# Kernel tuning notes

Hardware: AMD Instinct MI355X
Metric: run time of the kernel (lower is better)

Reference implementation:

```python
import jax, jax.numpy as jnp
import numpy as np

D_MODEL = 192
D_STATE = 16
D_CONV = 4
EXPAND = 2
HEADDIM = 16
D_INNER = EXPAND * D_MODEL          # 384
NHEADS = D_INNER // HEADDIM         # 24
NGROUPS = 1
CHUNK = 256
BATCH = 2
SEQLEN = 8192
D_IN_PROJ = 2 * D_INNER + NGROUPS * D_STATE + NHEADS   # 808
D_IN_PROJ_B = NGROUPS * D_STATE                         # 16
CONV_DIM = D_INNER + NGROUPS * D_STATE                  # 400
EPS = 1e-5


def silu(x):
    return x * jax.nn.sigmoid(x)


def causal_dwconv(x, w, b):
    # x: (B, L, C), w: (C, 1, K) depthwise, b: (C,). Causal: left-pad K-1.
    C = x.shape[-1]
    xt = jnp.transpose(x, (0, 2, 1))  # (B, C, L)
    y = jax.lax.conv_general_dilated(
        xt, w, window_strides=(1,), padding=[(D_CONV - 1, 0)],
        dimension_numbers=('NCH', 'OIH', 'NCH'), feature_group_count=C)
    return jnp.transpose(y + b[None, :, None], (0, 2, 1))


def segsum(x):
    # x: (..., T) -> (..., T, T) lower-triangular segment sums (exclusive of j, inclusive of i)
    T = x.shape[-1]
    cs = jnp.cumsum(x, axis=-1)
    seg = cs[..., :, None] - cs[..., None, :]
    mask = jnp.tril(jnp.ones((T, T), dtype=bool))
    return jnp.where(mask, seg, -jnp.inf)


def ssd(x, dt, A, Bm, Cm):
    # Mamba2 chunked selective scan (mamba_chunk_scan_combined semantics).
    # x:(b,l,h,p) dt:(b,l,h) A:(h,) Bm,Cm:(b,l,g,n)
    b, l, h, p = x.shape
    g = Bm.shape[2]
    Bm = jnp.repeat(Bm, h // g, axis=2)  # (b,l,h,n)
    Cm = jnp.repeat(Cm, h // g, axis=2)
    nchunks = l // CHUNK
    tochunk = lambda t: t.reshape(b, nchunks, CHUNK, *t.shape[2:])
    xc, dtc, Bc, Cc = map(tochunk, (x, dt, Bm, Cm))
    a = jnp.transpose(dtc * A, (0, 3, 1, 2))        # (b,h,c,cl)
    a_cum = jnp.cumsum(a, axis=-1)                   # (b,h,c,cl)
    Lmat = jnp.exp(segsum(a))                        # (b,h,c,cl,cl)
    xdt = xc * dtc[..., None]                        # (b,c,cl,h,p)
    # intra-chunk (diagonal) output
    Y_diag = jnp.einsum('bclhn,bcshn,bhcls,bcshp->bclhp', Cc, Bc, Lmat, xdt)
    # per-chunk end states
    decay_states = jnp.exp(a_cum[..., -1:] - a_cum)  # (b,h,c,cl)
    states = jnp.einsum('bclhn,bhcl,bclhp->bchpn', Bc, decay_states, xdt)
    # inter-chunk recurrence (associative, via chunk-level segsum)
    init = jnp.zeros_like(states[:, :1])
    states = jnp.concatenate([init, states], axis=1)              # (b,c+1,h,p,n)
    a_chunk = jnp.pad(a_cum[..., -1], ((0, 0), (0, 0), (1, 0)))   # (b,h,c+1)
    decay_chunk = jnp.exp(segsum(a_chunk))                        # (b,h,c+1,c+1)
    states = jnp.einsum('bhzc,bchpn->bzhpn', decay_chunk, states)[:, :-1]  # (b,c,h,p,n)
    # state -> output within each chunk
    Y_off = jnp.einsum('bclhn,bchpn,bhcl->bclhp', Cc, states, jnp.exp(a_cum))
    return (Y_diag + Y_off).reshape(b, l, h, p)


def setup_inputs() -> dict:
    key = jax.random.key(0)
    ks = jax.random.split(key, 12)
    rng = np.random.default_rng(0)
    u = jax.random.normal(ks[0], (BATCH, SEQLEN, D_MODEL), dtype=jnp.float32)
    support = jax.random.normal(ks[1], (BATCH, SEQLEN, D_MODEL), dtype=jnp.float32)
    W_in = jax.random.normal(ks[2], (D_IN_PROJ, D_MODEL), dtype=jnp.float32) * 0.02
    W_in_b = jax.random.normal(ks[3], (D_IN_PROJ_B, D_MODEL), dtype=jnp.float32) * 0.02
    conv_w = jax.random.normal(ks[4], (CONV_DIM, 1, D_CONV), dtype=jnp.float32) * 0.2
    conv_b = jnp.zeros((CONV_DIM,), dtype=jnp.float32)
    conv_w_b = jax.random.normal(ks[5], (D_IN_PROJ_B, 1, D_CONV), dtype=jnp.float32) * 0.2
    conv_b_b = jnp.zeros((D_IN_PROJ_B,), dtype=jnp.float32)
    # dt_bias init per the module (inverse-softplus of dt in [1e-3, 1e-1])
    dt = np.exp(rng.uniform(size=(NHEADS,)) * (np.log(0.1) - np.log(0.001)) + np.log(0.001))
    dt = np.clip(dt, 1e-4, None)
    dt_bias = jnp.asarray(dt + np.log(-np.expm1(-dt)), dtype=jnp.float32)
    A_log = jnp.asarray(np.log(rng.uniform(1.0, 16.0, size=(NHEADS,))), dtype=jnp.float32)
    D = jnp.ones((NHEADS,), dtype=jnp.float32)
    norm_w = jnp.ones((D_INNER,), dtype=jnp.float32)
    W_out = jax.random.normal(ks[6], (D_MODEL, D_INNER), dtype=jnp.float32) * 0.02
    return {'u': u, 'support': support, 'W_in': W_in, 'W_in_b': W_in_b,
            'conv_w': conv_w, 'conv_b': conv_b, 'conv_w_b': conv_w_b, 'conv_b_b': conv_b_b,
            'dt_bias': dt_bias, 'A_log': A_log, 'D': D, 'norm_w': norm_w, 'W_out': W_out}


def reference(u, support, W_in, W_in_b, conv_w, conv_b, conv_w_b, conv_b_b,
              dt_bias, A_log, D, norm_w, W_out):
    bsz, l, _ = u.shape
    zxbdt = u @ W_in.T                                  # (b,l,808)
    c = support @ W_in_b.T                              # (b,l,16)
    z = zxbdt[..., :D_INNER]
    xB = zxbdt[..., D_INNER:D_INNER + CONV_DIM]
    dt = jax.nn.softplus(zxbdt[..., -NHEADS:] + dt_bias)  # (b,l,h)
    A = -jnp.exp(A_log)
    xB = silu(causal_dwconv(xB, conv_w, conv_b))
    Cv = silu(causal_dwconv(c, conv_w_b, conv_b_b))
    x = xB[..., :D_INNER]
    Bv = xB[..., D_INNER:]
    xh = x.reshape(bsz, l, NHEADS, HEADDIM)
    Bg = Bv.reshape(bsz, l, NGROUPS, D_STATE)
    Cg = Cv.reshape(bsz, l, NGROUPS, D_STATE)
    y = ssd(xh, dt, A, Bg, Cg) + D[None, None, :, None] * xh
    y = y.reshape(bsz, l, D_INNER)
    # RMSNormGated, norm_before_gate=False: normalize(y * silu(z)) * weight
    yg = y * silu(z)
    yn = yg * jax.lax.rsqrt(jnp.mean(yg * yg, axis=-1, keepdims=True) + EPS) * norm_w
    return yn @ W_out.T
```

## Files before the change

### kernel.cpp

```cpp
#include <hip/hip_runtime.h>
#include <cmath>

#define ROWS      16384
#define SEQLEN    8192
#define BATCH     2
#define NHEADS    24
#define HEADDIM   16
#define D_STATE   16
#define D_INNER   384
#define D_MODEL   192
#define D_IN_PROJ 808
#define CONV_DIM  400
#define NCHUNKS   32
#define CHUNK     256
#define EPS       1e-5f
#define LOG2E     1.44269504088896f

typedef short bf16x8 __attribute__((ext_vector_type(8)));
typedef float f32x4  __attribute__((ext_vector_type(4)));
typedef unsigned short us4v __attribute__((ext_vector_type(4)));
typedef unsigned short us8v __attribute__((ext_vector_type(8)));

__device__ __forceinline__ float silu_f(float x) { return x / (1.0f + expf(-x)); }
__device__ __forceinline__ float softplus_f(float x) { return (x > 20.0f) ? x : log1pf(expf(x)); }
__device__ __forceinline__ unsigned short f2bf(float x) {
  unsigned u = __builtin_bit_cast(unsigned, x);
  u += 0x7fff + ((u >> 16) & 1);
  return (unsigned short)(u >> 16);
}
__device__ __forceinline__ float bf2f(unsigned short s) {
  unsigned u = (unsigned)s << 16;
  return __builtin_bit_cast(float, u);
}
__device__ __forceinline__ unsigned pk_bf(float a, float b) {
  unsigned ua = __builtin_bit_cast(unsigned, a) + 0x7fffu;
  unsigned ub = __builtin_bit_cast(unsigned, b) + 0x7fffu;
  return __builtin_amdgcn_perm(ub, ua, 0x07060302u);
}

__global__ __launch_bounds__(256)
void cvt3_kernel(const float* __restrict__ a, unsigned short* __restrict__ ao, long na,
                 const float* __restrict__ b, unsigned short* __restrict__ bo, long nb,
                 const float* __restrict__ c, unsigned short* __restrict__ co, long nc) {
  const long t0 = na >> 2, t1 = t0 + (nb >> 2), t2 = t1 + (nc >> 2);
  const long stride = (long)gridDim.x * blockDim.x;
  for (long i = (long)blockIdx.x * blockDim.x + threadIdx.x; i < t2; i += stride) {
    const float4* s; us4v* d; long j;
    if (i < t0)      { s = (const float4*)a; d = (us4v*)ao; j = i; }
    else if (i < t1) { s = (const float4*)b; d = (us4v*)bo; j = i - t0; }
    else             { s = (const float4*)c; d = (us4v*)co; j = i - t1; }
    float4 v = s[j];
    us4v o = { f2bf(v.x), f2bf(v.y), f2bf(v.z), f2bf(v.w) };
    d[j] = o;
  }
}

template<bool A_F32, bool OUT_BF16>
__launch_bounds__(256, 3)
__global__ void gemm_bf16(const void* __restrict__ Ap,
                          const unsigned short* __restrict__ W,
                          void* __restrict__ Cp, int M, int N, int K) {
  constexpr int BM = 128, BN = 128, BK = 32, LDK = 40;
  __shared__ unsigned short As[2][BM * LDK];
  __shared__ unsigned short Ws[2][BN * LDK];
  const int tid  = threadIdx.x;
  const int wid  = tid >> 6, lane = tid & 63;
  const int wr   = wid >> 1, wc = wid & 1;
  const int fr   = lane & 15, fq = lane >> 4;
  const long m0  = (long)blockIdx.y * BM;
  const int  n0  = blockIdx.x * BN;

  f32x4 acc[4][4] = {};

  auto stage = [&](int k0, int buf) {
    if (A_F32) {
      const float* A = (const float*)Ap;
#pragma unroll
      for (int p = 0; p < 2; ++p) {
        int flat = p * 2048 + tid * 8;
        int r = flat >> 5, c = flat & 31;
        const float4* src = (const float4*)(A + (m0 + r) * (long)K + k0 + c);
        float4 v0 = src[0], v1 = src[1];
        us8v o = { f2bf(v0.x), f2bf(v0.y), f2bf(v0.z), f2bf(v0.w),
                   f2bf(v1.x), f2bf(v1.y), f2bf(v1.z), f2bf(v1.w) };
        *(us8v*)&As[buf][r * LDK + c] = o;
      }
    } else {
      const unsigned short* A = (const unsigned short*)Ap;
#pragma unroll
      for (int p = 0; p < 2; ++p) {
        int flat = p * 2048 + tid * 8;
        int r = flat >> 5, c = flat & 31;
        us8v v = *(const us8v*)(A + (m0 + r) * (long)K + k0 + c);
        *(us8v*)&As[buf][r * LDK + c] = v;
      }
    }
#pragma unroll
    for (int p = 0; p < 2; ++p) {
      int flat = p * 2048 + tid * 8;
      int r = flat >> 5, c = flat & 31;
      int gn = n0 + r;
      us8v v = { 0, 0, 0, 0, 0, 0, 0, 0 };
      if (gn < N) v = *(const us8v*)(W + (long)gn * K + k0 + c);
      *(us8v*)&Ws[buf][r * LDK + c] = v;
    }
  };

  const int nk = K / BK;
  stage(0, 0);
  __syncthreads();
  for (int kt = 0; kt < nk; ++kt) {
    const int cur = kt & 1;
    if (kt + 1 < nk) stage((kt + 1) * BK, cur ^ 1);
    bf16x8 af[4], bfr[4];
#pragma unroll
    for (int m = 0; m < 4; ++m)
      af[m] = *(const bf16x8*)&As[cur][(wr * 64 + m * 16 + fr) * LDK + fq * 8];
#pragma unroll
    for (int n = 0; n < 4; ++n)
      bfr[n] = *(const bf16x8*)&Ws[cur][(wc * 64 + n * 16 + fr) * LDK + fq * 8];
#pragma unroll
    for (int m = 0; m < 4; ++m)
#pragma unroll
      for (int n = 0; n < 4; ++n)
        acc[m][n] = __builtin_amdgcn_mfma_f32_16x16x32_bf16(bfr[n], af[m], acc[m][n], 0, 0, 0);
    __syncthreads();
  }

#pragma unroll
  for (int m = 0; m < 4; ++m) {
    const long gm = m0 + wr * 64 + m * 16 + fr;
#pragma unroll
    for (int n = 0; n < 4; ++n) {
      const int gn = n0 + wc * 64 + n * 16 + fq * 4;
      if (gn < N) {
        if (OUT_BF16) {
          us4v o = { f2bf(acc[m][n][0]), f2bf(acc[m][n][1]),
                     f2bf(acc[m][n][2]), f2bf(acc[m][n][3]) };
          *(us4v*)((unsigned short*)Cp + gm * N + gn) = o;
        } else {
          float4 o = make_float4(acc[m][n][0], acc[m][n][1], acc[m][n][2], acc[m][n][3]);
          *(float4*)((float*)Cp + gm * N + gn) = o;
        }
      }
    }
  }
}

#define CBC_NB  (ROWS * 4 / 256)
#define CDT_NB  (ROWS * 3 / 256)

__global__ __launch_bounds__(256)
void conv_bcdt(const unsigned short* __restrict__ zxbdt, const float* __restrict__ cproj,
               const float* __restrict__ conv_w, const float* __restrict__ conv_b,
               const float* __restrict__ conv_w_b, const float* __restrict__ conv_b_b,
               const float* __restrict__ dt_bias,
               unsigned short* __restrict__ Bo, unsigned short* __restrict__ Co,
               float* __restrict__ dtoT) {
  const int blk = blockIdx.x;
  const us8v z8 = { 0, 0, 0, 0, 0, 0, 0, 0 };

  if (blk < CBC_NB) {
    const int idx = blk * 256 + threadIdx.x;
    const int row = idx / 4, q = idx % 4;
    const int b = row / SEQLEN, t = row % SEQLEN;

    if (q < 2) {
      const int c0 = q * 8;
      const unsigned short* base = zxbdt + (size_t)row * D_IN_PROJ + D_INNER + 384 + c0;
      us8v x0 = (t >= 3) ? *(const us8v*)(base - 3 * D_IN_PROJ) : z8;
      us8v x1 = (t >= 2) ? *(const us8v*)(base - 2 * D_IN_PROJ) : z8;
      us8v x2 = (t >= 1) ? *(const us8v*)(base - 1 * D_IN_PROJ) : z8;
      us8v x3 = *(const us8v*)base;
      us8v o;
#pragma unroll
      for (int ch = 0; ch < 8; ++ch) {
        const float4 wv = *(const float4*)(conv_w + (384 + c0 + ch) * 4);
        float acc = conv_b[384 + c0 + ch] + wv.x * bf2f(x0[ch]) + wv.y * bf2f(x1[ch])
                  + wv.z * bf2f(x2[ch]) + wv.w * bf2f(x3[ch]);
        o[ch] = f2bf(silu_f(acc));
      }
      *(us8v*)(Bo + (size_t)row * D_STATE + c0) = o;
    } else {
      const int c0 = (q - 2) * 8;
      const float* base = cproj + (size_t)row * D_STATE + c0;
      float c0r[8], c1r[8], c2r[8], c3r[8];
#pragma unroll
      for (int half = 0; half < 2; ++half) {
        float4 v0 = (t >= 3) ? *(const float4*)(base - 3 * D_STATE + 4 * half) : make_float4(0,0,0,0);
        float4 v1 = (t >= 2) ? *(const float4*)(base - 2 * D_STATE + 4 * half) : make_float4(0,0,0,0);
        float4 v2 = (t >= 1) ? *(const float4*)(base - 1 * D_STATE + 4 * half) : make_float4(0,0,0,0);
        float4 v3 = *(const float4*)(base + 4 * half);
        c0r[4*half+0]=v0.x; c0r[4*half+1]=v0.y; c0r[4*half+2]=v0.z; c0r[4*half+3]=v0.w;
        c1r[4*half+0]=v1.x; c1r[4*half+1]=v1.y; c1r[4*half+2]=v1.z; c1r[4*half+3]=v1.w;
        c2r[4*half+0]=v2.x; c2r[4*half+1]=v2.y; c2r[4*half+2]=v2.z; c2r[4*half+3]=v2.w;
        c3r[4*half+0]=v3.x; c3r[4*half+1]=v3.y; c3r[4*half+2]=v3.z; c3r[4*half+3]=v3.w;
      }
      us8v o;
#pragma unroll
      for (int ch = 0; ch < 8; ++ch) {
        const float4 wv = *(const float4*)(conv_w_b + (c0 + ch) * 4);
        float acc = conv_b_b[c0 + ch] + wv.x * c0r[ch] + wv.y * c1r[ch]
                  + wv.z * c2r[ch] + wv.w * c3r[ch];
        o[ch] = f2bf(silu_f(acc));
      }
      *(us8v*)(Co + (size_t)row * D_STATE + c0) = o;
    }
  } else {
    const int idx = (blk - CBC_NB) * 256 + threadIdx.x;
    const int row = idx / 3, q = idx % 3;
    const int b = row / SEQLEN, t = row % SEQLEN;
    const int h0 = q * 8;
    us8v dv = *(const us8v*)(zxbdt + (size_t)row * D_IN_PROJ + (D_IN_PROJ - NHEADS) + h0);
#pragma unroll
    for (int j = 0; j < 8; ++j) {
      float v = bf2f(dv[j]) + dt_bias[h0 + j];
      dtoT[(size_t)(b * NHEADS + h0 + j) * SEQLEN + t] = softplus_f(v);
    }
  }
}

__global__ __launch_bounds__(512, 4)
void ssd_mfma_kernel(const unsigned short* __restrict__ zxbdt, const unsigned short* __restrict__ Bo,
                     const unsigned short* __restrict__ Co, const float* __restrict__ dtoT,
                     const float* __restrict__ A_log, const float* __restrict__ conv_w,
                     const float* __restrict__ conv_b, const float* __restrict__ Dvec,
                     unsigned short* __restrict__ YdT, float* __restrict__ acum_g,
                     float* __restrict__ csum_g, float* __restrict__ stloc) {
  const int h    = blockIdx.x;
  const int cidx = blockIdx.y;
  const int b    = blockIdx.z;
  const int tid  = threadIdx.x;
  const int wid  = tid >> 6, lane = tid & 63;
  const int fr   = lane & 15, g = lane >> 4;

  __shared__ unsigned short Bs[256 * 24 + 32];
  __shared__ unsigned short xsT[16 * 264];
  __shared__ unsigned short BwT[16 * 264];
  __shared__ unsigned short Ps[8][16 * 40];
  __shared__ unsigned short xraw[259 * 16 + 8];
  __shared__ float sc[CHUNK];
  __shared__ float sc2[CHUNK];
  __shared__ float sred[2][256];
  __shared__ float wsum[4];

  const float Ah = -expf(A_log[h]);
  const us8v z8 = { 0, 0, 0, 0, 0, 0, 0, 0 };

  float v = 0.f;
  if (tid < CHUNK) {
    v = dtoT[(size_t)(b * NHEADS + h) * SEQLEN + (size_t)cidx * CHUNK + tid] * Ah;
#pragma unroll
    for (int off = 1; off < 64; off <<= 1) {
      float u = __shfl_up(v, off, 64);
      if (lane >= off) v += u;
    }
    if (lane == 63) wsum[wid] = v;
  }

  const int r  = tid >> 1;
  const int hf = tid & 1;
  const size_t rrow  = (size_t)b * SEQLEN + (size_t)cidx * CHUNK + r;
  const size_t rhrow = (size_t)(b * NHEADS + h) * SEQLEN + (size_t)cidx * CHUNK + r;
  const float rdtv = dtoT[rhrow];
  us8v bh = ((const us8v*)(Bo + rrow * D_STATE))[hf];
  *(us8v*)&Bs[r * 24 + 8 * hf] = bh;
  if (hf == 0) *(us8v*)&Bs[r * 24 + 16] = z8;
  if (tid < 32) Bs[256 * 24 + tid] = 0;
  {
    const int tg = cidx * CHUNK + r - 3;
    us8v xv = z8;
    if (tg >= 0)
      xv = *(const us8v*)(zxbdt + ((size_t)b * SEQLEN + tg) * D_IN_PROJ + D_INNER + h * HEADDIM + 8 * hf);
    *(us8v*)&xraw[r * 16 + 8 * hf] = xv;
    if (tid < 6) {
      const int rr2 = 256 + (tid >> 1);
      const int hf2 = tid & 1;
      const int tg2 = cidx * CHUNK + rr2 - 3;
      us8v xv2 = *(const us8v*)(zxbdt + ((size_t)b * SEQLEN + tg2) * D_IN_PROJ + D_INNER + h * HEADDIM + 8 * hf2);
      *(us8v*)&xraw[rr2 * 16 + 8 * hf2] = xv2;
    }
  }
  __syncthreads();

  us8v xsil, xdt8;
  {
    us8v tA = *(const us8v*)&xraw[(r + 0) * 16 + 8 * hf];
    us8v tB = *(const us8v*)&xraw[(r + 1) * 16 + 8 * hf];
    us8v tC = *(const us8v*)&xraw[(r + 2) * 16 + 8 * hf];
    us8v tD = *(const us8v*)&xraw[(r + 3) * 16 + 8 * hf];
    const int cbase = h * HEADDIM + 8 * hf;
#pragma unroll
    for (int ch = 0; ch < 8; ++ch) {
      const float4 wv = *(const float4*)(conv_w + (cbase + ch) * 4);
      float acc = conv_b[cbase + ch] + wv.x * bf2f(tA[ch]) + wv.y * bf2f(tB[ch])
                + wv.z * bf2f(tC[ch]) + wv.w * bf2f(tD[ch]);
      float sv = silu_f(acc);
      xsil[ch] = f2bf(sv);
      xdt8[ch] = f2bf(sv * rdtv);
    }
  }
  const float ctot = wsum[0] + wsum[1] + wsum[2] + wsum[3];
  if (tid < CHUNK) {
    float pre = 0.f;
#pragma unroll
    for (int w = 0; w < 4; ++w) if (w < wid) pre += wsum[w];
    v += pre;
    sc[tid]  = v;
    sc2[tid] = v * LOG2E;
    acum_g[(size_t)(b * NHEADS + h) * SEQLEN + (size_t)cidx * CHUNK + tid] = v;
    if (tid == CHUNK - 1) csum_g[(b * NHEADS + h) * NCHUNKS + cidx] = v;
  }
  __syncthreads();

  *(us8v*)&xraw[(r + 3) * 16 + 8 * hf] = xsil;
#pragma unroll
  for (int q = 0; q < 8; ++q)
    xsT[(q + 8 * hf) * 264 + r] = xdt8[q];
  {
    const float wdv = __expf(ctot - sc[r]);
#pragma unroll
    for (int q = 0; q < 8; ++q)
      BwT[(q + 8 * hf) * 264 + r] = f2bf(bf2f(bh[q]) * wdv);
  }
  __syncthreads();

  if (wid < 2) {
    f32x4 accS = {};
#pragma unroll
    for (int k2 = 0; k2 < 4; ++k2) {
      bf16x8 af = *(const bf16x8*)&BwT[fr * 264 + wid * 128 + 32 * k2 + 8 * g];
      bf16x8 bb = *(const bf16x8*)&xsT[fr * 264 + wid * 128 + 32 * k2 + 8 * g];
      accS = __builtin_amdgcn_mfma_f32_16x16x32_bf16(af, bb, accS, 0, 0, 0);
    }
    *(f32x4*)&sred[wid][fr * 16 + 4 * g] = accS;
  }

  const int strips[2] = { wid, 15 - wid };
  const f32x4 zf = { 0.f, 0.f, 0.f, 0.f };
  const unsigned short* Cbase = Co + ((size_t)b * SEQLEN + (size_t)cidx * CHUNK) * D_STATE;
  const float Dh = Dvec[h];
#pragma unroll
  for (int q = 0; q < 2; ++q) {
    const int lt = strips[q];
    f32x4 acc = zf;
    bf16x8 cf = { 0, 0, 0, 0, 0, 0, 0, 0 };
    if (g < 2) cf = *(const bf16x8*)(Cbase + (lt * 16 + fr) * D_STATE + 8 * g);
    const float acl2 = sc2[lt * 16 + fr];
    const int   lg   = lt * 16 + fr;
    const int npair = (lt + 2) >> 1;
    for (int sp = 0; sp < npair; ++sp) {
#pragma unroll
      for (int ti = 0; ti < 2; ++ti) {
        const int st = 2 * sp + ti;
        if (st < lt) {
          bf16x8 bfg = *(const bf16x8*)&Bs[(st * 16 + fr) * 24 + 8 * g];
          f32x4 G = __builtin_amdgcn_mfma_f32_16x16x32_bf16(bfg, cf, zf, 0, 0, 0);
          f32x4 se2 = *(const f32x4*)&sc2[st * 16 + 4 * g];
          float w0 = exp2f(acl2 - se2[0]);
          float w1 = exp2f(acl2 - se2[1]);
          float w2 = exp2f(acl2 - se2[2]);
          float w3 = exp2f(acl2 - se2[3]);
          uint2 pk;
          pk.x = pk_bf(G[0] * w0, G[1] * w1);
          pk.y = pk_bf(G[2] * w2, G[3] * w3);
          *(uint2*)&Ps[wid][fr * 40 + 16 * ti + 4 * g] = pk;
        } else if (st == lt) {
          bf16x8 bfg = *(const bf16x8*)&Bs[(st * 16 + fr) * 24 + 8 * g];
          f32x4 G = __builtin_amdgcn_mfma_f32_16x16x32_bf16(bfg, cf, zf, 0, 0, 0);
          f32x4 se2 = *(const f32x4*)&sc2[st * 16 + 4 * g];
          const int sbase = st * 16 + 4 * g;
          float w0 = (sbase + 0 <= lg) ? exp2f(acl2 - se2[0]) : 0.f;
          float w1 = (sbase + 1 <= lg) ? exp2f(acl2 - se2[1]) : 0.f;
          float w2 = (sbase + 2 <= lg) ? exp2f(acl2 - se2[2]) : 0.f;
          float w3 = (sbase + 3 <= lg) ? exp2f(acl2 - se2[3]) : 0.f;
          uint2 pk;
          pk.x = pk_bf(G[0] * w0, G[1] * w1);
          pk.y = pk_bf(G[2] * w2, G[3] * w3);
          *(uint2*)&Ps[wid][fr * 40 + 16 * ti + 4 * g] = pk;
        } else {
          uint2 zz; zz.x = 0u; zz.y = 0u;
          *(uint2*)&Ps[wid][fr * 40 + 16 * ti + 4 * g] = zz;
        }
      }
      const bf16x8 pf = *(const bf16x8*)&Ps[wid][fr * 40 + 8 * g];
      const bf16x8 xf = *(const bf16x8*)&xsT[fr * 264 + sp * 32 + 8 * g];
      acc = __builtin_amdgcn_mfma_f32_16x16x32_bf16(xf, pf, acc, 0, 0, 0);
    }
    us4v xs4 = *(const us4v*)&xraw[(lt * 16 + fr + 3) * 16 + 4 * g];
    us4v o = { f2bf(acc[0] + Dh * bf2f(xs4[0])),
               f2bf(acc[1] + Dh * bf2f(xs4[1])),
               f2bf(acc[2] + Dh * bf2f(xs4[2])),
               f2bf(acc[3] + Dh * bf2f(xs4[3])) };
    *(us4v*)(YdT + ((size_t)(b * NHEADS + h) * SEQLEN + (size_t)cidx * CHUNK + lt * 16 + fr) * HEADDIM
             + 4 * g) = o;
  }

  __syncthreads();
  if (tid < 256) {
    stloc[((size_t)(b * NCHUNKS + cidx) * NHEADS + h) * 256 + tid] = sred[0][tid] + sred[1][tid];
  }
}

__global__ __launch_bounds__(256)
void chunk_scan_kernel(const float* __restrict__ stloc, const float* __restrict__ csum_g,
                       float* __restrict__ stpre) {
  const int b  = blockIdx.x / NHEADS;
  const int h  = blockIdx.x % NHEADS;
  const int pn = threadIdx.x;
  float S = 0.0f;
  for (int c = 0; c < NCHUNKS; ++c) {
    const size_t idx = ((size_t)(b * NCHUNKS + c) * NHEADS + h) * 256 + pn;
    stpre[idx] = S;
    S = __expf(csum_g[(b * NHEADS + h) * NCHUNKS + c]) * S + stloc[idx];
  }
}

#define TT 16
__global__ __launch_bounds__(384)
void yoff_norm_tiled(const unsigned short* __restrict__ YdT,
                     const unsigned short* __restrict__ Co, const float* __restrict__ acum_g,
                     const float* __restrict__ stpre,
                     const unsigned short* __restrict__ zxbdt, const float* __restrict__ norm_w,
                     unsigned short* __restrict__ yn) {
  const int r0   = blockIdx.x * TT;
  const int b    = r0 / SEQLEN;
  const int t0   = r0 % SEQLEN;
  const int cidx = t0 / CHUNK;
  const int d    = threadIdx.x;
  const int h    = d >> 4, p = d & 15;
  const int wv   = d >> 6;

  __shared__ unsigned short Yt[NHEADS * TT * 16];
  __shared__ float At[NHEADS * TT];
  __shared__ float Ct[TT * 16];
  __shared__ float red[TT][6];

  {
    us8v* Yt8 = (us8v*)Yt;
#pragma unroll
    for (int rep = 0; rep < 2; ++rep) {
      int j = d + rep * 384;
      int hh = j >> 5, q = j & 31;
      const size_t src = ((size_t)(b * NHEADS + hh) * SEQLEN + t0) * HEADDIM + q * 8;
      Yt8[j] = *(const us8v*)(YdT + src);
    }
    At[d] = acum_g[(size_t)(b * NHEADS + (d >> 4)) * SEQLEN + t0 + (d & 15)];
    if (d < TT * 16) Ct[d] = bf2f(Co[(size_t)r0 * D_STATE + d]);
  }

  float S[16];
  {
    const float* Sp = stpre + ((size_t)(b * NCHUNKS + cidx) * NHEADS + h) * 256 + p * 16;
#pragma unroll
    for (int q = 0; q < 4; ++q) {
      float4 v4 = *(const float4*)(Sp + 4 * q);
      S[4 * q + 0] = v4.x; S[4 * q + 1] = v4.y; S[4 * q + 2] = v4.z; S[4 * q + 3] = v4.w;
    }
  }
  const float nw = norm_w[d];
  __syncthreads();

  float yg[TT];
#pragma unroll
  for (int tt = 0; tt < TT; ++tt) {
    float dot = 0.f;
#pragma unroll
    for (int n = 0; n < 16; ++n) dot += Ct[tt * 16 + n] * S[n];
    const float acl = At[h * TT + tt];
    float y = bf2f(Yt[h * 256 + tt * 16 + p]) + __expf(acl) * dot;
    const float z = bf2f(zxbdt[(size_t)(r0 + tt) * D_IN_PROJ + d]);
    yg[tt] = y * silu_f(z);
    float s = yg[tt] * yg[tt];
#pragma unroll
    for (int off = 32; off > 0; off >>= 1) s += __shfl_down(s, off);
    if ((d & 63) == 0) red[tt][wv] = s;
  }
  __syncthreads();

#pragma unroll
  for (int tt = 0; tt < TT; ++tt) {
    const float tot = red[tt][0] + red[tt][1] + red[tt][2] + red[tt][3] + red[tt][4] + red[tt][5];
    const float scale = rsqrtf(tot * (1.0f / D_INNER) + EPS);
    yn[(size_t)(r0 + tt) * D_INNER + d] = f2bf(yg[tt] * scale * nw);
  }
}

extern "C" void kernel_launch(void* const* d_in, const int* in_sizes, int n_in,
                              void* d_out, int out_size, void* d_ws, size_t ws_size,
                              hipStream_t stream) {
  const float* u        = (const float*)d_in[0];
  const float* support  = (const float*)d_in[1];
  const float* W_in     = (const float*)d_in[2];
  const float* W_in_b   = (const float*)d_in[3];
  const float* conv_w   = (const float*)d_in[4];
  const float* conv_b   = (const float*)d_in[5];
  const float* conv_w_b = (const float*)d_in[6];
  const float* conv_b_b = (const float*)d_in[7];
  const float* dt_bias  = (const float*)d_in[8];
  const float* A_log    = (const float*)d_in[9];
  const float* Dvec     = (const float*)d_in[10];
  const float* norm_w   = (const float*)d_in[11];
  const float* W_out    = (const float*)d_in[12];
  float* out = (float*)d_out;
  char* wsb  = (char*)d_ws;

  unsigned short* Wi_b  = (unsigned short*)(wsb);
  unsigned short* Wo_b  = Wi_b + (size_t)D_IN_PROJ * D_MODEL;
  unsigned short* Wib_b = Wo_b + (size_t)D_MODEL * D_INNER;
  unsigned short* zxbdt = Wib_b + (size_t)D_STATE * D_MODEL;
  unsigned short* Bo    = zxbdt + (size_t)ROWS * D_IN_PROJ;
  unsigned short* Co    = Bo + (size_t)ROWS * D_STATE;
  unsigned short* YdT   = Co + (size_t)ROWS * D_STATE;
  unsigned short* yn    = YdT + (size_t)ROWS * D_INNER;
  float* cproj = (float*)(yn + (size_t)ROWS * D_INNER);
  float* dtoT  = cproj + (size_t)ROWS * D_STATE;
  float* acum  = dtoT  + (size_t)ROWS * NHEADS;
  float* csum  = acum  + (size_t)BATCH * NHEADS * SEQLEN;
  float* stloc = csum  + (size_t)BATCH * NHEADS * NCHUNKS;
  float* stpre = stloc + (size_t)BATCH * NCHUNKS * NHEADS * 256;

  cvt3_kernel<<<224, 256, 0, stream>>>(W_in, Wi_b, (long)D_IN_PROJ * D_MODEL,
                                       W_out, Wo_b, (long)D_MODEL * D_INNER,
                                       W_in_b, Wib_b, (long)D_STATE * D_MODEL);
  gemm_bf16<true, true><<<dim3((D_IN_PROJ + 127) / 128, ROWS / 128), 256, 0, stream>>>(
      u, Wi_b, zxbdt, ROWS, D_IN_PROJ, D_MODEL);
  gemm_bf16<true, false><<<dim3(1, ROWS / 128), 256, 0, stream>>>(
      support, Wib_b, cproj, ROWS, D_STATE, D_MODEL);
  conv_bcdt<<<CBC_NB + CDT_NB, 256, 0, stream>>>(
      zxbdt, cproj, conv_w, conv_b, conv_w_b, conv_b_b, dt_bias, Bo, Co, dtoT);
  ssd_mfma_kernel<<<dim3(NHEADS, NCHUNKS, BATCH), 512, 0, stream>>>(
      zxbdt, Bo, Co, dtoT, A_log, conv_w, conv_b, Dvec, YdT, acum, csum, stloc);
  chunk_scan_kernel<<<BATCH * NHEADS, 256, 0, stream>>>(stloc, csum, stpre);
  yoff_norm_tiled<<<ROWS / TT, 384, 0, stream>>>(YdT, Co, acum, stpre, zxbdt, norm_w, yn);
  gemm_bf16<false, false><<<dim3((D_MODEL + 127) / 128, ROWS / 128), 256, 0, stream>>>(
      yn, Wo_b, out, ROWS, D_MODEL, D_INNER);
}
```

Before: 130.6 us.

## Route in-projection GEMM outputs into per-consumer layouts, store C projection in bf16

The in-projection GEMM epilogue now writes z, x, B and dt into separate buffers instead of one interleaved 808-wide row. x goes to a head-major (b,h,t,p) layout so the SSD kernel reads contiguous 16-element rows per head. The C projection GEMM now writes bf16 instead of fp32, and the conv kernel shares one code path for B and C. This aims to cut strided, poorly coalesced reads in downstream kernels. The cost is scattered, narrower stores in the GEMM epilogue and some extra branching there.

```diff
diff --git a/kernel.cpp b/kernel.cpp
--- a/kernel.cpp
+++ b/kernel.cpp
@@ -55,11 +55,15 @@
   }
 }
 
-template<bool A_F32, bool OUT_BF16>
+template<bool A_F32, bool OUT_BF16, bool ROUTE>
 __launch_bounds__(256, 3)
 __global__ void gemm_bf16(const void* __restrict__ Ap,
                           const unsigned short* __restrict__ W,
-                          void* __restrict__ Cp, int M, int N, int K) {
+                          void* __restrict__ Cp, int M, int N, int K,
+                          unsigned short* __restrict__ zbuf,
+                          unsigned short* __restrict__ xT,
+                          unsigned short* __restrict__ Braw,
+                          unsigned short* __restrict__ draw) {
   constexpr int BM = 128, BN = 128, BK = 32, LDK = 40;
   __shared__ unsigned short As[2][BM * LDK];
   __shared__ unsigned short Ws[2][BN * LDK];
@@ -134,7 +138,22 @@
     for (int n = 0; n < 4; ++n) {
       const int gn = n0 + wc * 64 + n * 16 + fq * 4;
       if (gn < N) {
-        if (OUT_BF16) {
+        if (ROUTE) {
+          us4v o = { f2bf(acc[m][n][0]), f2bf(acc[m][n][1]),
+                     f2bf(acc[m][n][2]), f2bf(acc[m][n][3]) };
+          const int bb = (int)(gm >> 13);
+          const long t = gm & 8191;
+          if (gn < 384) {
+            *(us4v*)(zbuf + gm * 384 + gn) = o;
+          } else if (gn < 768) {
+            const int c = gn - 384, hh = c >> 4, ii = c & 15;
+            *(us4v*)(xT + (((size_t)(bb * NHEADS + hh) * SEQLEN + t) << 4) + ii) = o;
+          } else if (gn < 784) {
+            *(us4v*)(Braw + gm * 16 + (gn - 768)) = o;
+          } else {
+            *(us4v*)(draw + gm * 24 + (gn - 784)) = o;
+          }
+        } else if (OUT_BF16) {
           us4v o = { f2bf(acc[m][n][0]), f2bf(acc[m][n][1]),
                      f2bf(acc[m][n][2]), f2bf(acc[m][n][3]) };
           *(us4v*)((unsigned short*)Cp + gm * N + gn) = o;
@@ -151,7 +170,8 @@
 #define CDT_NB  (ROWS * 3 / 256)
 
 __global__ __launch_bounds__(256)
-void conv_bcdt(const unsigned short* __restrict__ zxbdt, const float* __restrict__ cproj,
+void conv_bcdt(const unsigned short* __restrict__ Braw, const unsigned short* __restrict__ craw,
+               const unsigned short* __restrict__ draw,
                const float* __restrict__ conv_w, const float* __restrict__ conv_b,
                const float* __restrict__ conv_w_b, const float* __restrict__ conv_b_b,
                const float* __restrict__ dt_bias,
@@ -165,53 +185,31 @@
     const int row = idx / 4, q = idx % 4;
     const int b = row / SEQLEN, t = row % SEQLEN;
 
-    if (q < 2) {
-      const int c0 = q * 8;
-      const unsigned short* base = zxbdt + (size_t)row * D_IN_PROJ + D_INNER + 384 + c0;
-      us8v x0 = (t >= 3) ? *(const us8v*)(base - 3 * D_IN_PROJ) : z8;
-      us8v x1 = (t >= 2) ? *(const us8v*)(base - 2 * D_IN_PROJ) : z8;
-      us8v x2 = (t >= 1) ? *(const us8v*)(base - 1 * D_IN_PROJ) : z8;
-      us8v x3 = *(const us8v*)base;
-      us8v o;
-#pragma unroll
-      for (int ch = 0; ch < 8; ++ch) {
-        const float4 wv = *(const float4*)(conv_w + (384 + c0 + ch) * 4);
-        float acc = conv_b[384 + c0 + ch] + wv.x * bf2f(x0[ch]) + wv.y * bf2f(x1[ch])
-                  + wv.z * bf2f(x2[ch]) + wv.w * bf2f(x3[ch]);
-        o[ch] = f2bf(silu_f(acc));
-      }
-      *(us8v*)(Bo + (size_t)row * D_STATE + c0) = o;
-    } else {
-      const int c0 = (q - 2) * 8;
-      const float* base = cproj + (size_t)row * D_STATE + c0;
-      float c0r[8], c1r[8], c2r[8], c3r[8];
-#pragma unroll
-      for (int half = 0; half < 2; ++half) {
-        float4 v0 = (t >= 3) ? *(const float4*)(base - 3 * D_STATE + 4 * half) : make_float4(0,0,0,0);
-        float4 v1 = (t >= 2) ? *(const float4*)(base - 2 * D_STATE + 4 * half) : make_float4(0,0,0,0);
-        float4 v2 = (t >= 1) ? *(const float4*)(base - 1 * D_STATE + 4 * half) : make_float4(0,0,0,0);
-        float4 v3 = *(const float4*)(base + 4 * half);
-        c0r[4*half+0]=v0.x; c0r[4*half+1]=v0.y; c0r[4*half+2]=v0.z; c0r[4*half+3]=v0.w;
-        c1r[4*half+0]=v1.x; c1r[4*half+1]=v1.y; c1r[4*half+2]=v1.z; c1r[4*half+3]=v1.w;
-        c2r[4*half+0]=v2.x; c2r[4*half+1]=v2.y; c2r[4*half+2]=v2.z; c2r[4*half+3]=v2.w;
-        c3r[4*half+0]=v3.x; c3r[4*half+1]=v3.y; c3r[4*half+2]=v3.z; c3r[4*half+3]=v3.w;
-      }
-      us8v o;
-#pragma unroll
-      for (int ch = 0; ch < 8; ++ch) {
-        const float4 wv = *(const float4*)(conv_w_b + (c0 + ch) * 4);
-        float acc = conv_b_b[c0 + ch] + wv.x * c0r[ch] + wv.y * c1r[ch]
-                  + wv.z * c2r[ch] + wv.w * c3r[ch];
-        o[ch] = f2bf(silu_f(acc));
-      }
-      *(us8v*)(Co + (size_t)row * D_STATE + c0) = o;
-    }
+    const unsigned short* src = (q < 2) ? Braw : craw;
+    const float* cw = (q < 2) ? conv_w + 384 * 4 : conv_w_b;
+    const float* cb = (q < 2) ? conv_b + 384 : conv_b_b;
+    const int c0 = (q & 1) * 8;
+    const unsigned short* base = src + (size_t)row * D_STATE + c0;
+    us8v x0 = (t >= 3) ? *(const us8v*)(base - 3 * D_STATE) : z8;
+    us8v x1 = (t >= 2) ? *(const us8v*)(base - 2 * D_STATE) : z8;
+    us8v x2 = (t >= 1) ? *(const us8v*)(base - 1 * D_STATE) : z8;
+    us8v x3 = *(const us8v*)base;
+    us8v o;
+#pragma unroll
+    for (int ch = 0; ch < 8; ++ch) {
+      const float4 wv = *(const float4*)(cw + (c0 + ch) * 4);
+      float acc = cb[c0 + ch] + wv.x * bf2f(x0[ch]) + wv.y * bf2f(x1[ch])
+                + wv.z * bf2f(x2[ch]) + wv.w * bf2f(x3[ch]);
+      o[ch] = f2bf(silu_f(acc));
+    }
+    if (q < 2) *(us8v*)(Bo + (size_t)row * D_STATE + c0) = o;
+    else       *(us8v*)(Co + (size_t)row * D_STATE + c0) = o;
   } else {
     const int idx = (blk - CBC_NB) * 256 + threadIdx.x;
     const int row = idx / 3, q = idx % 3;
     const int b = row / SEQLEN, t = row % SEQLEN;
     const int h0 = q * 8;
-    us8v dv = *(const us8v*)(zxbdt + (size_t)row * D_IN_PROJ + (D_IN_PROJ - NHEADS) + h0);
+    us8v dv = *(const us8v*)(draw + (size_t)row * 24 + h0);
 #pragma unroll
     for (int j = 0; j < 8; ++j) {
       float v = bf2f(dv[j]) + dt_bias[h0 + j];
@@ -221,7 +219,7 @@
 }
 
 __global__ __launch_bounds__(512, 4)
-void ssd_mfma_kernel(const unsigned short* __restrict__ zxbdt, const unsigned short* __restrict__ Bo,
+void ssd_mfma_kernel(const unsigned short* __restrict__ xT, const unsigned short* __restrict__ Bo,
                      const unsigned short* __restrict__ Co, const float* __restrict__ dtoT,
                      const float* __restrict__ A_log, const float* __restrict__ conv_w,
                      const float* __restrict__ conv_b, const float* __restrict__ Dvec,
@@ -271,13 +269,13 @@
     const int tg = cidx * CHUNK + r - 3;
     us8v xv = z8;
     if (tg >= 0)
-      xv = *(const us8v*)(zxbdt + ((size_t)b * SEQLEN + tg) * D_IN_PROJ + D_INNER + h * HEADDIM + 8 * hf);
+      xv = *(const us8v*)(xT + (((size_t)(b * NHEADS + h) * SEQLEN + tg) << 4) + 8 * hf);
     *(us8v*)&xraw[r * 16 + 8 * hf] = xv;
     if (tid < 6) {
       const int rr2 = 256 + (tid >> 1);
       const int hf2 = tid & 1;
       const int tg2 = cidx * CHUNK + rr2 - 3;
-      us8v xv2 = *(const us8v*)(zxbdt + ((size_t)b * SEQLEN + tg2) * D_IN_PROJ + D_INNER + h * HEADDIM + 8 * hf2);
+      us8v xv2 = *(const us8v*)(xT + (((size_t)(b * NHEADS + h) * SEQLEN + tg2) << 4) + 8 * hf2);
       *(us8v*)&xraw[rr2 * 16 + 8 * hf2] = xv2;
     }
   }
@@ -421,7 +419,7 @@
 void yoff_norm_tiled(const unsigned short* __restrict__ YdT,
                      const unsigned short* __restrict__ Co, const float* __restrict__ acum_g,
                      const float* __restrict__ stpre,
-                     const unsigned short* __restrict__ zxbdt, const float* __restrict__ norm_w,
+                     const unsigned short* __restrict__ zbuf, const float* __restrict__ norm_w,
                      unsigned short* __restrict__ yn) {
   const int r0   = blockIdx.x * TT;
   const int b    = r0 / SEQLEN;
@@ -469,7 +467,7 @@
     for (int n = 0; n < 16; ++n) dot += Ct[tt * 16 + n] * S[n];
     const float acl = At[h * TT + tt];
     float y = bf2f(Yt[h * 256 + tt * 16 + p]) + __expf(acl) * dot;
-    const float z = bf2f(zxbdt[(size_t)(r0 + tt) * D_IN_PROJ + d]);
+    const float z = bf2f(zbuf[(size_t)(r0 + tt) * 384 + d]);
     yg[tt] = y * silu_f(z);
     float s = yg[tt] * yg[tt];
 #pragma unroll
@@ -508,13 +506,16 @@
   unsigned short* Wi_b  = (unsigned short*)(wsb);
   unsigned short* Wo_b  = Wi_b + (size_t)D_IN_PROJ * D_MODEL;
   unsigned short* Wib_b = Wo_b + (size_t)D_MODEL * D_INNER;
-  unsigned short* zxbdt = Wib_b + (size_t)D_STATE * D_MODEL;
-  unsigned short* Bo    = zxbdt + (size_t)ROWS * D_IN_PROJ;
+  unsigned short* zbuf  = Wib_b + (size_t)D_STATE * D_MODEL;
+  unsigned short* xT    = zbuf + (size_t)ROWS * D_INNER;
+  unsigned short* Braw  = xT + (size_t)ROWS * D_INNER;
+  unsigned short* draw  = Braw + (size_t)ROWS * D_STATE;
+  unsigned short* craw  = draw + (size_t)ROWS * NHEADS;
+  unsigned short* Bo    = craw + (size_t)ROWS * D_STATE;
   unsigned short* Co    = Bo + (size_t)ROWS * D_STATE;
   unsigned short* YdT   = Co + (size_t)ROWS * D_STATE;
   unsigned short* yn    = YdT + (size_t)ROWS * D_INNER;
-  float* cproj = (float*)(yn + (size_t)ROWS * D_INNER);
-  float* dtoT  = cproj + (size_t)ROWS * D_STATE;
+  float* dtoT  = (float*)(yn + (size_t)ROWS * D_INNER);
   float* acum  = dtoT  + (size_t)ROWS * NHEADS;
   float* csum  = acum  + (size_t)BATCH * NHEADS * SEQLEN;
   float* stloc = csum  + (size_t)BATCH * NHEADS * NCHUNKS;
@@ -523,16 +524,16 @@
   cvt3_kernel<<<224, 256, 0, stream>>>(W_in, Wi_b, (long)D_IN_PROJ * D_MODEL,
                                        W_out, Wo_b, (long)D_MODEL * D_INNER,
                                        W_in_b, Wib_b, (long)D_STATE * D_MODEL);
-  gemm_bf16<true, true><<<dim3((D_IN_PROJ + 127) / 128, ROWS / 128), 256, 0, stream>>>(
-      u, Wi_b, zxbdt, ROWS, D_IN_PROJ, D_MODEL);
-  gemm_bf16<true, false><<<dim3(1, ROWS / 128), 256, 0, stream>>>(
-      support, Wib_b, cproj, ROWS, D_STATE, D_MODEL);
+  gemm_bf16<true, true, true><<<dim3(7, ROWS / 128), 256, 0, stream>>>(
+      u, Wi_b, nullptr, ROWS, D_IN_PROJ, D_MODEL, zbuf, xT, Braw, draw);
+  gemm_bf16<true, true, false><<<dim3(1, ROWS / 128), 256, 0, stream>>>(
+      support, Wib_b, craw, ROWS, D_STATE, D_MODEL, nullptr, nullptr, nullptr, nullptr);
   conv_bcdt<<<CBC_NB + CDT_NB, 256, 0, stream>>>(
-      zxbdt, cproj, conv_w, conv_b, conv_w_b, conv_b_b, dt_bias, Bo, Co, dtoT);
+      Braw, craw, draw, conv_w, conv_b, conv_w_b, conv_b_b, dt_bias, Bo, Co, dtoT);
   ssd_mfma_kernel<<<dim3(NHEADS, NCHUNKS, BATCH), 512, 0, stream>>>(
-      zxbdt, Bo, Co, dtoT, A_log, conv_w, conv_b, Dvec, YdT, acum, csum, stloc);
+      xT, Bo, Co, dtoT, A_log, conv_w, conv_b, Dvec, YdT, acum, csum, stloc);
   chunk_scan_kernel<<<BATCH * NHEADS, 256, 0, stream>>>(stloc, csum, stpre);
-  yoff_norm_tiled<<<ROWS / TT, 384, 0, stream>>>(YdT, Co, acum, stpre, zxbdt, norm_w, yn);
-  gemm_bf16<false, false><<<dim3((D_MODEL + 127) / 128, ROWS / 128), 256, 0, stream>>>(
-      yn, Wo_b, out, ROWS, D_MODEL, D_INNER);
-}
+  yoff_norm_tiled<<<ROWS / TT, 384, 0, stream>>>(YdT, Co, acum, stpre, zbuf, norm_w, yn);
+  gemm_bf16<false, false, false><<<dim3((D_MODEL + 127) / 128, ROWS / 128), 256, 0, stream>>>(
+      yn, Wo_b, out, ROWS, D_MODEL, D_INNER, nullptr, nullptr, nullptr, nullptr);
+}
```

Result: no change. 128.7 us (-1.4%).
